# Performance work log

Measured on AMD Instinct MI355X. Metric: run time of the kernel, lower is better.

The kernel has to match this reference:

```python
import jax, jax.numpy as jnp
import numpy as np

B, C, L = 32, 128, 4096          # batch, n_channels, signal length
P, Q = 100, 20                   # n_projections, n_quantiles


def setup_inputs() -> dict:
    key = jax.random.key(0)
    k1, k2, k3, k4 = jax.random.split(key, 4)
    X = jax.random.normal(k1, (B, C, L), dtype=jnp.float32)
    # conv1d kernel of shape (P, C, 1) collapsed to (P, C)
    W = jax.random.normal(k2, (P, C), dtype=jnp.float32)
    s = 2.33 * jnp.sqrt(jnp.float32(C))
    min_vals = -s + 0.1 * jax.random.normal(k3, (P,), dtype=jnp.float32)
    max_vals = s + 0.1 * jax.random.normal(k4, (P,), dtype=jnp.float32)
    return {"X": X, "W": W, "min_vals": min_vals, "max_vals": max_vals}


def reference(X, W, min_vals, max_vals):
    # kernel-size-1 conv1d == channel projection
    a = jnp.einsum('bcl,pc->bpl', X, W)  # [B, P, L]
    fracs = jnp.arange(1, Q + 1, dtype=a.dtype) / jnp.asarray(Q + 1, a.dtype)
    thr = min_vals[None, :] + (max_vals - min_vals)[None, :] * fracs[:, None]  # [Q, P]

    def body(carry, t):  # t: [P] thresholds for one quantile
        cdf_q = jnp.mean((a < t[None, :, None]).astype(a.dtype), axis=-1)  # [B, P]
        return carry, cdf_q

    _, cdf = jax.lax.scan(body, None, thr)          # [Q, B, P]
    cdf = jnp.transpose(cdf, (1, 2, 0))             # [B, P, Q]
    return cdf.reshape(B, P * Q)
```

## Files before the change

kernel.cpp:

```cpp
#include <hip/hip_runtime.h>
#include <hip/hip_bf16.h>

#define B_    32
#define C_    128
#define L_    4096
#define P_    100
#define NPT   7
#define Q_    20
#define NBIN  21
#define NCH   (NPT * 4)
#define CHS   512
#define TPB   1024
#define LSPAN 512

typedef short          bf16x8 __attribute__((ext_vector_type(8)));
typedef float          f32x4  __attribute__((ext_vector_type(4)));
typedef unsigned short u16x8  __attribute__((ext_vector_type(8)));

__device__ inline unsigned short f2bf(float f) {
    __hip_bfloat16 h = __float2bfloat16(f);
    unsigned short u; __builtin_memcpy(&u, &h, 2);
    return u;
}

__global__ void prep_w_kernel(const float* __restrict__ W, unsigned short* __restrict__ Wf) {
    const int t = blockIdx.x * 256 + threadIdx.x;
    if (t >= NCH * 64) return;
    const int chunk = t >> 6, lane = t & 63;
    const int pt = chunk >> 2, ks = chunk & 3;
    const int p  = pt * 16 + (lane & 15);
    const int c0 = ks * 32 + (lane >> 4) * 8;
    u16x8 v;
#pragma unroll
    for (int j = 0; j < 8; ++j)
        v[j] = (p < P_) ? f2bf(W[p * C_ + c0 + j]) : (unsigned short)0;
    *(u16x8*)(Wf + (size_t)t * 8) = v;
}

__global__ __launch_bounds__(TPB, 4)
void radon_mfma5_kernel(const float* __restrict__ X, const unsigned short* __restrict__ Wf,
                        const float* __restrict__ minv, const float* __restrict__ maxv,
                        float* __restrict__ out) {
    __shared__ unsigned short Wlds[NCH * CHS];
    __shared__ int   hist[P_ * NBIN];
    __shared__ float mn_s[P_], invd_s[P_];

    const int tid  = threadIdx.x;
    const int b    = blockIdx.y;
    const int lblk = blockIdx.x;
    const int wave = tid >> 6;
    const int lane = tid & 63;
    const int quad = lane >> 4;
    const int nn   = lane & 15;

    {
        const int4* src = (const int4*)Wf;
        int4* dst = (int4*)Wlds;
        for (int k = tid; k < NCH * 64; k += TPB)
            dst[k] = src[k];
    }
    for (int i = tid; i < P_; i += TPB) {
        const float mn = minv[i];
        mn_s[i]   = mn;
        invd_s[i] = (float)NBIN / (maxv[i] - mn);
    }
    for (int i = tid; i < P_ * NBIN; i += TPB) hist[i] = 0;
    __syncthreads();

    const int l0 = lblk * LSPAN + wave * 32;
    const float* Xb = X + (size_t)b * C_ * L_;
    float xv[2][4][8];
#pragma unroll
    for (int lt = 0; lt < 2; ++lt)
#pragma unroll
        for (int ks = 0; ks < 4; ++ks)
#pragma unroll
            for (int j = 0; j < 8; ++j)
                xv[lt][ks][j] = Xb[(size_t)(ks * 32 + quad * 8 + j) * L_ + l0 + lt * 16 + nn];

    bf16x8 bfrag[2][4];
#pragma unroll
    for (int lt = 0; lt < 2; ++lt)
#pragma unroll
        for (int ks = 0; ks < 4; ++ks) {
            unsigned int u[4];
#pragma unroll
            for (int jp = 0; jp < 4; ++jp) {
                __hip_bfloat162 h2 = __float22bfloat162_rn(
                    make_float2(xv[lt][ks][2 * jp], xv[lt][ks][2 * jp + 1]));
                __builtin_memcpy(&u[jp], &h2, 4);
            }
            __builtin_memcpy(&bfrag[lt][ks], u, 16);
        }

    for (int pt = 0; pt < NPT; ++pt) {
        bf16x8 afrag[4];
#pragma unroll
        for (int ks = 0; ks < 4; ++ks)
            afrag[ks] = *(const bf16x8*)(&Wlds[((pt * 4 + ks) * 64 + lane) * 8]);

        f32x4 acc0 = {0.f, 0.f, 0.f, 0.f};
        f32x4 acc1 = {0.f, 0.f, 0.f, 0.f};
#pragma unroll
        for (int ks = 0; ks < 4; ++ks) {
            acc0 = __builtin_amdgcn_mfma_f32_16x16x32_bf16(bfrag[0][ks], afrag[ks], acc0, 0, 0, 0);
            acc1 = __builtin_amdgcn_mfma_f32_16x16x32_bf16(bfrag[1][ks], afrag[ks], acc1, 0, 0, 0);
        }

        const int p = pt * 16 + nn;
        if (p < P_) {
            const float mn = mn_s[p], invd = invd_s[p];
            int* __restrict__ hrow = &hist[p * NBIN];
#pragma unroll
            for (int r = 0; r < 4; ++r) {
                {
                    const float t = (acc0[r] - mn) * invd;
                    int k = 0;
                    if (t > 0.f) { const int ki = (int)t; k = (ki > 20) ? 20 : ki; }
                    atomicAdd(&hrow[k], 1);
                }
                {
                    const float t = (acc1[r] - mn) * invd;
                    int k = 0;
                    if (t > 0.f) { const int ki = (int)t; k = (ki > 20) ? 20 : ki; }
                    atomicAdd(&hrow[k], 1);
                }
            }
        }
    }
    __syncthreads();

    for (int i = tid; i < P_ * Q_; i += TPB) {
        const int p  = i / Q_;
        const int qi = i - p * Q_;
        int s = 0;
        for (int k = 0; k <= qi; ++k) s += hist[p * NBIN + k];
        atomicAdd(&out[((size_t)b * P_ + p) * Q_ + qi], (float)s * (1.0f / (float)L_));
    }
}

extern "C" void kernel_launch(void* const* d_in, const int* in_sizes, int n_in,
                              void* d_out, int out_size, void* d_ws, size_t ws_size,
                              hipStream_t stream) {
    const float* X  = (const float*)d_in[0];
    const float* W  = (const float*)d_in[1];
    const float* mn = (const float*)d_in[2];
    const float* mx = (const float*)d_in[3];
    float* out = (float*)d_out;
    unsigned short* Wf = (unsigned short*)d_ws;

    hipMemsetAsync(out, 0, (size_t)out_size * sizeof(float), stream);
    prep_w_kernel<<<NCH * 64 / 256, 256, 0, stream>>>(W, Wf);

    dim3 grid(L_ / LSPAN, B_);
    radon_mfma5_kernel<<<grid, dim3(TPB), 0, stream>>>(X, Wf, mn, mx, out);
}
```

Baseline: 104.9 us.

## Software-pipeline X loads across K-steps with all projection accumulators live

```diff
diff --git a/kernel.cpp b/kernel.cpp
--- a/kernel.cpp
+++ b/kernel.cpp
@@ -12,6 +12,7 @@
 #define CHS   512
 #define TPB   1024
 #define LSPAN 512
+#define HSZ   (P_ * NBIN)
 
 typedef short          bf16x8 __attribute__((ext_vector_type(8)));
 typedef float          f32x4  __attribute__((ext_vector_type(4)));
@@ -38,11 +39,11 @@
 }
 
 __global__ __launch_bounds__(TPB, 4)
-void radon_mfma5_kernel(const float* __restrict__ X, const unsigned short* __restrict__ Wf,
+void radon_mfma7_kernel(const float* __restrict__ X, const unsigned short* __restrict__ Wf,
                         const float* __restrict__ minv, const float* __restrict__ maxv,
                         float* __restrict__ out) {
     __shared__ unsigned short Wlds[NCH * CHS];
-    __shared__ int   hist[P_ * NBIN];
+    __shared__ int   hist[HSZ];
     __shared__ float mn_s[P_], invd_s[P_];
 
     const int tid  = threadIdx.x;
@@ -64,49 +65,64 @@
         mn_s[i]   = mn;
         invd_s[i] = (float)NBIN / (maxv[i] - mn);
     }
-    for (int i = tid; i < P_ * NBIN; i += TPB) hist[i] = 0;
+    for (int i = tid; i < HSZ; i += TPB) hist[i] = 0;
     __syncthreads();
 
     const int l0 = lblk * LSPAN + wave * 32;
-    const float* Xb = X + (size_t)b * C_ * L_;
-    float xv[2][4][8];
+    const float* Xb = X + (size_t)b * C_ * L_ + l0 + nn;
+
+    f32x4 acc0[NPT], acc1[NPT];
 #pragma unroll
-    for (int lt = 0; lt < 2; ++lt)
+    for (int pt = 0; pt < NPT; ++pt) {
+        acc0[pt] = (f32x4){0.f, 0.f, 0.f, 0.f};
+        acc1[pt] = (f32x4){0.f, 0.f, 0.f, 0.f};
+    }
+
+    float xf[4][2][8];
 #pragma unroll
-        for (int ks = 0; ks < 4; ++ks)
+    for (int j = 0; j < 8; ++j) xf[0][0][j] = Xb[(size_t)(quad * 8 + j) * L_];
+#pragma unroll
+    for (int j = 0; j < 8; ++j) xf[0][1][j] = Xb[(size_t)(quad * 8 + j) * L_ + 16];
+
+#pragma unroll
+    for (int ks = 0; ks < 4; ++ks) {
+        __builtin_amdgcn_sched_barrier(0);
+        if (ks < 3) {
 #pragma unroll
             for (int j = 0; j < 8; ++j)
-                xv[lt][ks][j] = Xb[(size_t)(ks * 32 + quad * 8 + j) * L_ + l0 + lt * 16 + nn];
-
-    bf16x8 bfrag[2][4];
+                xf[ks + 1][0][j] = Xb[(size_t)((ks + 1) * 32 + quad * 8 + j) * L_];
 #pragma unroll
-    for (int lt = 0; lt < 2; ++lt)
-#pragma unroll
-        for (int ks = 0; ks < 4; ++ks) {
+            for (int j = 0; j < 8; ++j)
+                xf[ks + 1][1][j] = Xb[(size_t)((ks + 1) * 32 + quad * 8 + j) * L_ + 16];
+        }
+        bf16x8 b0, b1;
+        {
             unsigned int u[4];
 #pragma unroll
             for (int jp = 0; jp < 4; ++jp) {
                 __hip_bfloat162 h2 = __float22bfloat162_rn(
-                    make_float2(xv[lt][ks][2 * jp], xv[lt][ks][2 * jp + 1]));
+                    make_float2(xf[ks][0][2 * jp], xf[ks][0][2 * jp + 1]));
                 __builtin_memcpy(&u[jp], &h2, 4);
             }
-            __builtin_memcpy(&bfrag[lt][ks], u, 16);
+            __builtin_memcpy(&b0, u, 16);
+#pragma unroll
+            for (int jp = 0; jp < 4; ++jp) {
+                __hip_bfloat162 h2 = __float22bfloat162_rn(
+                    make_float2(xf[ks][1][2 * jp], xf[ks][1][2 * jp + 1]));
+                __builtin_memcpy(&u[jp], &h2, 4);
+            }
+            __builtin_memcpy(&b1, u, 16);
         }
+#pragma unroll
+        for (int pt = 0; pt < NPT; ++pt) {
+            bf16x8 a = *(const bf16x8*)(&Wlds[((pt * 4 + ks) * 64 + lane) * 8]);
+            acc0[pt] = __builtin_amdgcn_mfma_f32_16x16x32_bf16(b0, a, acc0[pt], 0, 0, 0);
+            acc1[pt] = __builtin_amdgcn_mfma_f32_16x16x32_bf16(b1, a, acc1[pt], 0, 0, 0);
+        }
+    }
 
+#pragma unroll
     for (int pt = 0; pt < NPT; ++pt) {
-        bf16x8 afrag[4];
-#pragma unroll
-        for (int ks = 0; ks < 4; ++ks)
-            afrag[ks] = *(const bf16x8*)(&Wlds[((pt * 4 + ks) * 64 + lane) * 8]);
-
-        f32x4 acc0 = {0.f, 0.f, 0.f, 0.f};
-        f32x4 acc1 = {0.f, 0.f, 0.f, 0.f};
-#pragma unroll
-        for (int ks = 0; ks < 4; ++ks) {
-            acc0 = __builtin_amdgcn_mfma_f32_16x16x32_bf16(bfrag[0][ks], afrag[ks], acc0, 0, 0, 0);
-            acc1 = __builtin_amdgcn_mfma_f32_16x16x32_bf16(bfrag[1][ks], afrag[ks], acc1, 0, 0, 0);
-        }
-
         const int p = pt * 16 + nn;
         if (p < P_) {
             const float mn = mn_s[p], invd = invd_s[p];
@@ -114,13 +130,13 @@
 #pragma unroll
             for (int r = 0; r < 4; ++r) {
                 {
-                    const float t = (acc0[r] - mn) * invd;
+                    const float t = (acc0[pt][r] - mn) * invd;
                     int k = 0;
                     if (t > 0.f) { const int ki = (int)t; k = (ki > 20) ? 20 : ki; }
                     atomicAdd(&hrow[k], 1);
                 }
                 {
-                    const float t = (acc1[r] - mn) * invd;
+                    const float t = (acc1[pt][r] - mn) * invd;
                     int k = 0;
                     if (t > 0.f) { const int ki = (int)t; k = (ki > 20) ? 20 : ki; }
                     atomicAdd(&hrow[k], 1);
@@ -153,5 +169,5 @@
     prep_w_kernel<<<NCH * 64 / 256, 256, 0, stream>>>(W, Wf);
 
     dim3 grid(L_ / LSPAN, B_);
-    radon_mfma5_kernel<<<grid, dim3(TPB), 0, stream>>>(X, Wf, mn, mx, out);
+    radon_mfma7_kernel<<<grid, dim3(TPB), 0, stream>>>(X, Wf, mn, mx, out);
 }
```

Result: no change. 106.1 us (+1.1%).
